# Kernel optimization log

Hardware: AMD Instinct MI355X
Metric: run time of the kernel (lower is better)

## Reference

```python
import jax, jax.numpy as jnp
import numpy as np

B, T, C = 4, 4096, 1024


def setup_inputs() -> dict:
    key = jax.random.key(0)
    k_x, k_f, k_g, k_p = jax.random.split(key, 4)
    scale = 1.0 / np.sqrt(C)  # keep gate pre-activations well-scaled
    return {
        "x": jax.random.normal(k_x, (B, T, C), dtype=jnp.float32),
        "W_f_x": jax.random.normal(k_f, (C, C), dtype=jnp.float32) * scale,
        "W_g_x": jax.random.normal(k_g, (C, C), dtype=jnp.float32) * scale,
        "W_proj": jax.random.normal(k_p, (C, C), dtype=jnp.float32) * scale,
    }


def _cfc_scan(a, b):
    """Solve h_t = a_t * h_{t-1} + b_t with h_{-1}=0 along axis 1 (T).

    Associative op on linear maps: (A_l,B_l) then (A_r,B_r) composes to
    (A_r*A_l, A_r*B_l + B_r). With h_init=0, h_t = B-component.
    """
    def op(l, r):
        al, bl = l
        ar, br = r
        return ar * al, ar * bl + br
    _, h = jax.lax.associative_scan(op, (a, b), axis=1)
    return h


def reference(x, W_f_x, W_g_x, W_proj):
    # Gates depend on x only (parallel mode). nn.Linear: x @ W.T
    f = jax.nn.sigmoid(jnp.einsum("btc,dc->btd", x, W_f_x))  # (B,T,C)
    g = jnp.tanh(jnp.einsum("btc,dc->btd", x, W_g_x))        # (B,T,C)
    h = _cfc_scan(f, (1.0 - f) * g)                           # (B,T,C)
    return jnp.einsum("btc,dc->btd", h, W_proj)               # c_proj
```

## Files before the change

kernel.cpp:

```cpp
#include <hip/hip_runtime.h>
#include <hip/hip_bf16.h>
#include <stdint.h>

#define TT 4096
#define BB 4
#define CC 1024
#define MM (BB * TT)
#define NCHUNK 128
#define CHUNK_T (TT / NCHUNK)
#define NCHAIN (BB * CC)

typedef float f32x4 __attribute__((ext_vector_type(4)));
typedef __bf16 bf16x8 __attribute__((ext_vector_type(8)));

__device__ __forceinline__ float b2f(ushort u) {
  union { float f; uint32_t v; } x; x.v = ((uint32_t)u) << 16; return x.f;
}
__device__ __forceinline__ ushort f2b(float f) {
  union { float f; uint32_t u; } x; x.f = f;
  uint32_t r = x.u + 0x7fffu + ((x.u >> 16) & 1u);
  return (ushort)(r >> 16);
}

__device__ __forceinline__ void async_copy16(const ushort* g, ushort* l) {
  __builtin_amdgcn_global_load_lds(
      (__attribute__((address_space(1))) void*)(g),
      (__attribute__((address_space(3))) void*)(l), 16, 0, 0);
}

__global__ __launch_bounds__(256) void cvt_all(const float* __restrict__ x,
                                               const float* __restrict__ wf,
                                               const float* __restrict__ wg,
                                               const float* __restrict__ wp,
                                               ushort* __restrict__ xb,
                                               ushort* __restrict__ wcat,
                                               ushort* __restrict__ wpb) {
  const int i = blockIdx.x * 256 + threadIdx.x;
  const float* s; ushort* d; int off;
  if (i < 4194304)            { s = x;  d = xb;              off = i; }
  else if (i < 4456448)       { s = wf; d = wcat;            off = i - 4194304; }
  else if (i < 4718592)       { s = wg; d = wcat + 1048576;  off = i - 4456448; }
  else                        { s = wp; d = wpb;             off = i - 4718592; }
  float4 v = ((const float4*)s)[off];
  ushort4 o;
  o.x = f2b(v.x); o.y = f2b(v.y); o.z = f2b(v.z); o.w = f2b(v.w);
  ((ushort4*)d)[off] = o;
}


#define RDA(sl, ih)                                                       \
  _Pragma("unroll") for (int i_ = 0; i_ < 4; ++i_)                        \
      af[i_] = *(const bf16x8*)(rA + (sl) * 8192 + (ih) * 2048 + i_ * 512);

#define RDB(sl)                                                           \
  _Pragma("unroll") for (int j_ = 0; j_ < 4; ++j_)                        \
      bfr[j_] = *(const bf16x8*)(rB + (sl) * 8192 + j_ * 512);

#define MFMA16(ih)                                                        \
  __builtin_amdgcn_s_setprio(1);                                          \
  _Pragma("unroll") for (int i_ = 0; i_ < 4; ++i_)                        \
  _Pragma("unroll") for (int j_ = 0; j_ < 4; ++j_)                        \
      acc[(ih) * 4 + i_][j_] = __builtin_amdgcn_mfma_f32_16x16x32_bf16(   \
          bfr[j_], af[i_], acc[(ih) * 4 + i_][j_], 0, 0, 0);              \
  __builtin_amdgcn_s_setprio(0)

#define MIDBAR()                                                          \
  __builtin_amdgcn_s_barrier();                                           \
  asm volatile("s_waitcnt lgkmcnt(0)" ::: "memory");                      \
  __builtin_amdgcn_sched_barrier(0)

#define ENDBAR()                                                          \
  __builtin_amdgcn_s_barrier();                                           \
  __builtin_amdgcn_sched_barrier(0)

#define CK4() asm volatile("s_waitcnt vmcnt(4)" ::: "memory")
#define CK0() asm volatile("s_waitcnt vmcnt(0)" ::: "memory")

#define TILE(S0, S1, NS0, NS1, KN)                                        \
  RDA(S0, 0); RDB(S0); stageA(NS0, (KN));      MIDBAR(); MFMA16(0);        ENDBAR(); \
  RDA(S0, 1);          stageB(NS0, (KN));      MIDBAR(); MFMA16(1); CK4(); ENDBAR(); \
  RDA(S1, 0); RDB(S1); stageA(NS1, (KN) + 32); MIDBAR(); MFMA16(0);        ENDBAR(); \
  RDA(S1, 1);          stageB(NS1, (KN) + 32); MIDBAR(); MFMA16(1); CK4(); ENDBAR();

template <int MODE>
__global__ __launch_bounds__(512, 2) void gemm_bt(const ushort* __restrict__ A,
                                                  const ushort* __restrict__ Bw,
                                                  float* __restrict__ outF,
                                                  ushort* __restrict__ outB, int N) {
  constexpr int K = CC;
  __shared__ __align__(16) ushort sA[4 * 256 * 32];
  __shared__ __align__(16) ushort sB[4 * 256 * 32];

  const int tid = threadIdx.x;
  const int lane = tid & 63;
  const int w = tid >> 6;
  const int wm = w >> 2;
  const int wn = w & 3;

  const int nbx = N >> 8;
  const int cpx = (int)gridDim.x >> 3;
  const int bid = blockIdx.x;
  const int wg = (bid & 7) * cpx + (bid >> 3);
  const long n0 = (long)(wg % nbx) << 8;
  const long m0 = (long)(wg / nbx) << 8;

  const int srow = lane >> 2;
  const int goct = (lane & 3) ^ ((lane >> 3) & 3);
  const ushort* gA0 = A + (m0 + w * 16 + srow) * K + goct * 8;
  const ushort* gB0 = Bw + (n0 + w * 16 + srow) * K + goct * 8;
  const ushort* gA1 = gA0 + 128 * (long)K;
  const ushort* gB1 = gB0 + 128 * (long)K;
  ushort* dA0 = &sA[w * 512 + lane * 8];
  ushort* dA1 = dA0 + 4096;
  ushort* dB0 = &sB[w * 512 + lane * 8];
  ushort* dB1 = dB0 + 4096;

  auto stageA = [&](int slot, int koff) {
    async_copy16(gA0 + koff, dA0 + slot * 8192);
    async_copy16(gA1 + koff, dA1 + slot * 8192);
  };
  auto stageB = [&](int slot, int koff) {
    async_copy16(gB0 + koff, dB0 + slot * 8192);
    async_copy16(gB1 + koff, dB1 + slot * 8192);
  };

  const int rlo = lane & 15;
  const int kq = lane >> 4;
  const int oslot = kq ^ ((rlo >> 1) & 3);
  const ushort* rA = &sA[(wm * 128 + rlo) * 32 + oslot * 8];
  const ushort* rB = &sB[(wn * 64 + rlo) * 32 + oslot * 8];

  f32x4 acc[8][4];
#pragma unroll
  for (int i = 0; i < 8; ++i)
#pragma unroll
    for (int j = 0; j < 4; ++j) acc[i][j] = (f32x4){0.f, 0.f, 0.f, 0.f};

  bf16x8 af[4], bfr[4];

  stageA(0, 0);
  stageB(0, 0);
  stageA(1, 32);
  stageB(1, 32);
  CK4();
  ENDBAR();

  for (int t2 = 0; t2 < 7; ++t2) {
    const int kn = t2 * 128 + 64;
    TILE(0, 1, 2, 3, kn);
    TILE(2, 3, 0, 1, kn + 64);
  }
  TILE(0, 1, 2, 3, 960);
  RDA(2, 0); RDB(2); MIDBAR(); MFMA16(0); ENDBAR();
  RDA(2, 1);         MIDBAR(); MFMA16(1); CK0(); ENDBAR();
  RDA(3, 0); RDB(3); MIDBAR(); MFMA16(0); ENDBAR();
  RDA(3, 1);         MIDBAR(); MFMA16(1);

  const int mloc = lane & 15;
  const int nq = (lane >> 4) * 4;
#pragma unroll
  for (int i = 0; i < 8; ++i) {
    const long m = m0 + wm * 128 + i * 16 + mloc;
#pragma unroll
    for (int j = 0; j < 4; ++j) {
      const long nb = n0 + wn * 64 + j * 16 + nq;
      const f32x4 v = acc[i][j];
      if (MODE == 0) {
        *(f32x4*)(outF + m * N + nb) = v;
      } else {
        float act[4];
        if (n0 < CC) {
#pragma unroll
          for (int r = 0; r < 4; ++r)
            act[r] = __builtin_amdgcn_rcpf(1.f + __expf(-v[r]));
        } else {
#pragma unroll
          for (int r = 0; r < 4; ++r)
            act[r] = fmaf(-2.f, __builtin_amdgcn_rcpf(1.f + __expf(2.f * v[r])), 1.f);
        }
        ushort4 o;
        o.x = f2b(act[0]); o.y = f2b(act[1]); o.z = f2b(act[2]); o.w = f2b(act[3]);
        *(ushort4*)(outB + m * (long)N + nb) = o;
      }
    }
  }
}

__global__ __launch_bounds__(256) void scan_pass1(const ushort* __restrict__ P,
                                                  float* __restrict__ cA,
                                                  float* __restrict__ cB) {
  const int pc = blockIdx.x * 256 + threadIdx.x;
  const int chunk = blockIdx.y;
  const int b = pc >> 8, c4 = (pc & 255) * 4;
  const ushort4* p =
      (const ushort4*)(P + (size_t)(b * TT + chunk * CHUNK_T) * (2 * CC) + c4);
  float A[4] = {1.f, 1.f, 1.f, 1.f};
  float h[4] = {0.f, 0.f, 0.f, 0.f};
#pragma unroll 4
  for (int i = 0; i < CHUNK_T; ++i) {
    const ushort4 fu = p[0];
    const ushort4 gu = p[CC / 4];
    p += 2 * CC / 4;
    const float f[4] = {b2f(fu.x), b2f(fu.y), b2f(fu.z), b2f(fu.w)};
    const float g[4] = {b2f(gu.x), b2f(gu.y), b2f(gu.z), b2f(gu.w)};
#pragma unroll
    for (int r = 0; r < 4; ++r) {
      A[r] *= f[r];
      h[r] = fmaf(f[r], h[r], (1.f - f[r]) * g[r]);
    }
  }
  const int ci = chunk * NCHAIN + b * CC + c4;
  *(f32x4*)(cA + ci) = (f32x4){A[0], A[1], A[2], A[3]};
  *(f32x4*)(cB + ci) = (f32x4){h[0], h[1], h[2], h[3]};
}

__global__ __launch_bounds__(256) void scan_pass2(const float* __restrict__ cA,
                                                  const float* __restrict__ cB,
                                                  float* __restrict__ hinit) {
  const int chain = blockIdx.x * 256 + threadIdx.x;
  float h = 0.f;
  for (int j = 0; j < NCHUNK; ++j) {
    hinit[j * NCHAIN + chain] = h;
    h = fmaf(cA[j * NCHAIN + chain], h, cB[j * NCHAIN + chain]);
  }
}

__global__ __launch_bounds__(256) void scan_pass3(const ushort* __restrict__ P,
                                                  const float* __restrict__ hinit,
                                                  ushort* __restrict__ H) {
  const int pc = blockIdx.x * 256 + threadIdx.x;
  const int chunk = blockIdx.y;
  const int b = pc >> 8, c4 = (pc & 255) * 4;
  f32x4 hv = *(const f32x4*)(hinit + chunk * NCHAIN + b * CC + c4);
  float h[4] = {hv[0], hv[1], hv[2], hv[3]};
  const ushort4* p =
      (const ushort4*)(P + (size_t)(b * TT + chunk * CHUNK_T) * (2 * CC) + c4);
  ushort4* hp = (ushort4*)(H + (size_t)(b * TT + chunk * CHUNK_T) * CC + c4);
#pragma unroll 4
  for (int i = 0; i < CHUNK_T; ++i) {
    const ushort4 fu = p[0];
    const ushort4 gu = p[CC / 4];
    p += 2 * CC / 4;
    const float f[4] = {b2f(fu.x), b2f(fu.y), b2f(fu.z), b2f(fu.w)};
    const float g[4] = {b2f(gu.x), b2f(gu.y), b2f(gu.z), b2f(gu.w)};
    ushort4 o;
#pragma unroll
    for (int r = 0; r < 4; ++r)
      h[r] = fmaf(f[r], h[r], (1.f - f[r]) * g[r]);
    o.x = f2b(h[0]); o.y = f2b(h[1]); o.z = f2b(h[2]); o.w = f2b(h[3]);
    *hp = o;
    hp += CC / 4;
  }
}

extern "C" void kernel_launch(void* const* d_in, const int* in_sizes, int n_in,
                              void* d_out, int out_size, void* d_ws, size_t ws_size,
                              hipStream_t stream) {
  const float* x  = (const float*)d_in[0];
  const float* Wf = (const float*)d_in[1];
  const float* Wg = (const float*)d_in[2];
  const float* Wp = (const float*)d_in[3];

  char* ws = (char*)d_ws;
  ushort* xb   = (ushort*)(ws);
  ushort* Hb   = xb;
  ushort* Wcat = (ushort*)(ws + 33554432);
  ushort* Wpb  = (ushort*)(ws + 33554432 + 4194304);
  ushort* P    = (ushort*)(ws + 33554432 + 4194304 + 2097152);
  char* tail   = ws + 33554432 + 4194304 + 2097152 + 67108864;
  float* cA    = (float*)Wcat;
  float* cB    = (float*)(((char*)Wcat) + 2097152);
  float* hinit = (float*)(tail);
  (void)ws_size; (void)in_sizes; (void)n_in; (void)out_size;

  cvt_all<<<19456, 256, 0, stream>>>(x, Wf, Wg, Wp, xb, Wcat, Wpb);

  gemm_bt<1><<<512, 512, 0, stream>>>(xb, Wcat, nullptr, P, 2 * CC);

  dim3 gs(NCHAIN / 4 / 256, NCHUNK);
  scan_pass1<<<gs, 256, 0, stream>>>(P, cA, cB);
  scan_pass2<<<NCHAIN / 256, 256, 0, stream>>>(cA, cB, hinit);
  scan_pass3<<<gs, 256, 0, stream>>>(P, hinit, Hb);

  gemm_bt<0><<<256, 512, 0, stream>>>(Hb, Wpb, (float*)d_out, nullptr, CC);
}
```

Before: 280.7 us.

## Fuse chunk scan summaries into gate GEMM epilogue with interleaved f/g layout

Interleaves the f and g weight rows so each GEMM output tile holds matching f/g pairs per channel. The GEMM epilogue then computes per-chunk (A,B) scan summaries via wave shuffles, which removes the separate scan_pass1 read of the full gate tensor. pass2 becomes a 64-lane shuffle scan over chunks, and pass3 reads the interleaved f/g pairs with one 16-byte load. The cost is a heavier GEMM epilogue with many shuffles and strided small stores of the summaries.

After: 269.9 us. -3.8%, faster.

```diff
diff --git a/kernel.cpp b/kernel.cpp
--- a/kernel.cpp
+++ b/kernel.cpp
@@ -6,12 +6,13 @@
 #define BB 4
 #define CC 1024
 #define MM (BB * TT)
-#define NCHUNK 128
+#define NCHUNK 64
 #define CHUNK_T (TT / NCHUNK)
 #define NCHAIN (BB * CC)
 
 typedef float f32x4 __attribute__((ext_vector_type(4)));
 typedef __bf16 bf16x8 __attribute__((ext_vector_type(8)));
+typedef ushort us8 __attribute__((ext_vector_type(8)));
 
 __device__ __forceinline__ float b2f(ushort u) {
   union { float f; uint32_t v; } x; x.v = ((uint32_t)u) << 16; return x.f;
@@ -36,15 +37,22 @@
                                                ushort* __restrict__ wcat,
                                                ushort* __restrict__ wpb) {
   const int i = blockIdx.x * 256 + threadIdx.x;
-  const float* s; ushort* d; int off;
-  if (i < 4194304)            { s = x;  d = xb;              off = i; }
-  else if (i < 4456448)       { s = wf; d = wcat;            off = i - 4194304; }
-  else if (i < 4718592)       { s = wg; d = wcat + 1048576;  off = i - 4456448; }
-  else                        { s = wp; d = wpb;             off = i - 4718592; }
+  const float* s; ushort* d; int off, dst;
+  if (i < 4194304) {
+    s = x; d = xb; off = i; dst = i;
+  } else if (i < 4456448) {
+    s = wf; d = wcat; off = i - 4194304;
+    dst = ((off >> 8) << 9) + (off & 255);
+  } else if (i < 4718592) {
+    s = wg; d = wcat; off = i - 4456448;
+    dst = ((off >> 8) << 9) + 256 + (off & 255);
+  } else {
+    s = wp; d = wpb; off = i - 4718592; dst = off;
+  }
   float4 v = ((const float4*)s)[off];
   ushort4 o;
   o.x = f2b(v.x); o.y = f2b(v.y); o.z = f2b(v.z); o.w = f2b(v.w);
-  ((ushort4*)d)[off] = o;
+  ((ushort4*)d)[dst] = o;
 }
 
 
@@ -82,11 +90,21 @@
   RDA(S1, 0); RDB(S1); stageA(NS1, (KN) + 32); MIDBAR(); MFMA16(0);        ENDBAR(); \
   RDA(S1, 1);          stageB(NS1, (KN) + 32); MIDBAR(); MFMA16(1); CK4(); ENDBAR();
 
+#define BFLY16(Av, Bv)                                                    \
+  _Pragma("unroll") for (int m_ = 1; m_ < 16; m_ <<= 1) {                 \
+    float Ao_ = __shfl_xor(Av, m_);                                       \
+    float Bo_ = __shfl_xor(Bv, m_);                                       \
+    Bv = ((lane & m_) == 0) ? fmaf(Ao_, Bv, Bo_) : fmaf(Av, Bo_, Bv);     \
+    Av = Ao_ * Av;                                                        \
+  }
+
 template <int MODE>
 __global__ __launch_bounds__(512, 2) void gemm_bt(const ushort* __restrict__ A,
                                                   const ushort* __restrict__ Bw,
                                                   float* __restrict__ outF,
-                                                  ushort* __restrict__ outB, int N) {
+                                                  ushort* __restrict__ outB,
+                                                  float* __restrict__ cA2,
+                                                  float* __restrict__ cB2, int N) {
   constexpr int K = CC;
   __shared__ __align__(16) ushort sA[4 * 256 * 32];
   __shared__ __align__(16) ushort sB[4 * 256 * 32];
@@ -158,95 +176,110 @@
 
   const int mloc = lane & 15;
   const int nq = (lane >> 4) * 4;
-#pragma unroll
-  for (int i = 0; i < 8; ++i) {
-    const long m = m0 + wm * 128 + i * 16 + mloc;
-#pragma unroll
-    for (int j = 0; j < 4; ++j) {
-      const long nb = n0 + wn * 64 + j * 16 + nq;
-      const f32x4 v = acc[i][j];
-      if (MODE == 0) {
-        *(f32x4*)(outF + m * N + nb) = v;
-      } else {
-        float act[4];
-        if (n0 < CC) {
-#pragma unroll
-          for (int r = 0; r < 4; ++r)
-            act[r] = __builtin_amdgcn_rcpf(1.f + __expf(-v[r]));
-        } else {
-#pragma unroll
-          for (int r = 0; r < 4; ++r)
-            act[r] = fmaf(-2.f, __builtin_amdgcn_rcpf(1.f + __expf(2.f * v[r])), 1.f);
-        }
-        ushort4 o;
-        o.x = f2b(act[0]); o.y = f2b(act[1]); o.z = f2b(act[2]); o.w = f2b(act[3]);
-        *(ushort4*)(outB + m * (long)N + nb) = o;
+
+  if (MODE == 0) {
+#pragma unroll
+    for (int i = 0; i < 8; ++i) {
+      const long m = m0 + wm * 128 + i * 16 + mloc;
+#pragma unroll
+      for (int j = 0; j < 4; ++j) {
+        const long nb = n0 + wn * 64 + j * 16 + nq;
+        *(f32x4*)(outF + m * N + nb) = acc[i][j];
       }
     }
-  }
-}
-
-__global__ __launch_bounds__(256) void scan_pass1(const ushort* __restrict__ P,
-                                                  float* __restrict__ cA,
-                                                  float* __restrict__ cB) {
-  const int pc = blockIdx.x * 256 + threadIdx.x;
-  const int chunk = blockIdx.y;
-  const int b = pc >> 8, c4 = (pc & 255) * 4;
-  const ushort4* p =
-      (const ushort4*)(P + (size_t)(b * TT + chunk * CHUNK_T) * (2 * CC) + c4);
-  float A[4] = {1.f, 1.f, 1.f, 1.f};
-  float h[4] = {0.f, 0.f, 0.f, 0.f};
-#pragma unroll 4
-  for (int i = 0; i < CHUNK_T; ++i) {
-    const ushort4 fu = p[0];
-    const ushort4 gu = p[CC / 4];
-    p += 2 * CC / 4;
-    const float f[4] = {b2f(fu.x), b2f(fu.y), b2f(fu.z), b2f(fu.w)};
-    const float g[4] = {b2f(gu.x), b2f(gu.y), b2f(gu.z), b2f(gu.w)};
-#pragma unroll
-    for (int r = 0; r < 4; ++r) {
-      A[r] *= f[r];
-      h[r] = fmaf(f[r], h[r], (1.f - f[r]) * g[r]);
+  } else {
+    const int kq4 = lane >> 4;
+    const long bIdx = m0 >> 12;
+    const int t0 = (int)(m0 & 4095) + wm * 128;
+    const long chb = (n0 >> 1) + wn * 32;
+#pragma unroll
+    for (int cp = 0; cp < 2; ++cp) {
+      float CA[4][2], CB[4][2];
+#pragma unroll
+      for (int hh = 0; hh < 4; ++hh) {
+        const int i = cp * 4 + hh;
+        const long m = m0 + wm * 128 + i * 16 + mloc;
+#pragma unroll
+        for (int j = 0; j < 4; ++j) {
+          const long nb = n0 + wn * 64 + j * 16 + nq;
+          const f32x4 v = acc[i][j];
+          float act0 = __builtin_amdgcn_rcpf(1.f + __expf(-v[0]));
+          float act1 = fmaf(-2.f, __builtin_amdgcn_rcpf(1.f + __expf(2.f * v[1])), 1.f);
+          float act2 = __builtin_amdgcn_rcpf(1.f + __expf(-v[2]));
+          float act3 = fmaf(-2.f, __builtin_amdgcn_rcpf(1.f + __expf(2.f * v[3])), 1.f);
+          ushort4 o;
+          o.x = f2b(act0); o.y = f2b(act1); o.z = f2b(act2); o.w = f2b(act3);
+          *(ushort4*)(outB + m * (long)N + nb) = o;
+          const float fr0 = b2f(o.x), gr0 = b2f(o.y);
+          const float fr1 = b2f(o.z), gr1 = b2f(o.w);
+          float a0 = fr0, b0 = (1.f - fr0) * gr0;
+          float a1 = fr1, b1 = (1.f - fr1) * gr1;
+          BFLY16(a0, b0);
+          BFLY16(a1, b1);
+          if (hh == 0) {
+            CA[j][0] = a0; CB[j][0] = b0;
+            CA[j][1] = a1; CB[j][1] = b1;
+          } else {
+            CB[j][0] = fmaf(a0, CB[j][0], b0); CA[j][0] *= a0;
+            CB[j][1] = fmaf(a1, CB[j][1], b1); CA[j][1] *= a1;
+          }
+        }
+      }
+      if (mloc == 0) {
+        const int gchunk = (t0 >> 6) + cp;
+#pragma unroll
+        for (int j = 0; j < 4; ++j) {
+          const long ch0 = chb + j * 8 + kq4 * 2;
+          const long i0 = (bIdx * CC + ch0) * 64 + gchunk;
+          cA2[i0] = CA[j][0];       cB2[i0] = CB[j][0];
+          cA2[i0 + 64] = CA[j][1];  cB2[i0 + 64] = CB[j][1];
+        }
+      }
     }
   }
-  const int ci = chunk * NCHAIN + b * CC + c4;
-  *(f32x4*)(cA + ci) = (f32x4){A[0], A[1], A[2], A[3]};
-  *(f32x4*)(cB + ci) = (f32x4){h[0], h[1], h[2], h[3]};
-}
-
-__global__ __launch_bounds__(256) void scan_pass2(const float* __restrict__ cA,
-                                                  const float* __restrict__ cB,
-                                                  float* __restrict__ hinit) {
-  const int chain = blockIdx.x * 256 + threadIdx.x;
-  float h = 0.f;
-  for (int j = 0; j < NCHUNK; ++j) {
-    hinit[j * NCHAIN + chain] = h;
-    h = fmaf(cA[j * NCHAIN + chain], h, cB[j * NCHAIN + chain]);
-  }
+}
+
+__global__ __launch_bounds__(256) void scan_pass2(const float* __restrict__ cA2,
+                                                  const float* __restrict__ cB2,
+                                                  float* __restrict__ h2) {
+  const int gid = blockIdx.x * 256 + threadIdx.x;
+  const int chain = gid >> 6;
+  const int lane = threadIdx.x & 63;
+  float Av = cA2[chain * 64 + lane];
+  float Bv = cB2[chain * 64 + lane];
+#pragma unroll
+  for (int m = 1; m < 64; m <<= 1) {
+    const float Ao = __shfl_up(Av, m);
+    const float Bo = __shfl_up(Bv, m);
+    if (lane >= m) { Bv = fmaf(Av, Bo, Bv); Av = Av * Ao; }
+  }
+  const float Bx = __shfl_up(Bv, 1);
+  h2[chain * 64 + lane] = (lane == 0) ? 0.f : Bx;
 }
 
 __global__ __launch_bounds__(256) void scan_pass3(const ushort* __restrict__ P,
-                                                  const float* __restrict__ hinit,
+                                                  const float* __restrict__ h2,
                                                   ushort* __restrict__ H) {
   const int pc = blockIdx.x * 256 + threadIdx.x;
   const int chunk = blockIdx.y;
   const int b = pc >> 8, c4 = (pc & 255) * 4;
-  f32x4 hv = *(const f32x4*)(hinit + chunk * NCHAIN + b * CC + c4);
-  float h[4] = {hv[0], hv[1], hv[2], hv[3]};
-  const ushort4* p =
-      (const ushort4*)(P + (size_t)(b * TT + chunk * CHUNK_T) * (2 * CC) + c4);
+  float h[4];
+#pragma unroll
+  for (int r = 0; r < 4; ++r) h[r] = h2[(b * CC + c4 + r) * 64 + chunk];
+  const us8* p =
+      (const us8*)(P + (size_t)(b * TT + chunk * CHUNK_T) * (2 * CC) + c4 * 2);
   ushort4* hp = (ushort4*)(H + (size_t)(b * TT + chunk * CHUNK_T) * CC + c4);
 #pragma unroll 4
   for (int i = 0; i < CHUNK_T; ++i) {
-    const ushort4 fu = p[0];
-    const ushort4 gu = p[CC / 4];
-    p += 2 * CC / 4;
-    const float f[4] = {b2f(fu.x), b2f(fu.y), b2f(fu.z), b2f(fu.w)};
-    const float g[4] = {b2f(gu.x), b2f(gu.y), b2f(gu.z), b2f(gu.w)};
+    const us8 v = p[0];
+    p += 2 * CC / 8;
     ushort4 o;
 #pragma unroll
-    for (int r = 0; r < 4; ++r)
-      h[r] = fmaf(f[r], h[r], (1.f - f[r]) * g[r]);
+    for (int r = 0; r < 4; ++r) {
+      const float f = b2f(v[2 * r]);
+      const float g = b2f(v[2 * r + 1]);
+      h[r] = fmaf(f, h[r], (1.f - f) * g);
+    }
     o.x = f2b(h[0]); o.y = f2b(h[1]); o.z = f2b(h[2]); o.w = f2b(h[3]);
     *hp = o;
     hp += CC / 4;
@@ -268,19 +301,18 @@
   ushort* Wpb  = (ushort*)(ws + 33554432 + 4194304);
   ushort* P    = (ushort*)(ws + 33554432 + 4194304 + 2097152);
   char* tail   = ws + 33554432 + 4194304 + 2097152 + 67108864;
-  float* cA    = (float*)Wcat;
-  float* cB    = (float*)(((char*)Wcat) + 2097152);
-  float* hinit = (float*)(tail);
+  float* cA2   = (float*)(tail);
+  float* cB2   = (float*)(tail + 1048576);
+  float* h2    = (float*)(tail + 2097152);
   (void)ws_size; (void)in_sizes; (void)n_in; (void)out_size;
 
   cvt_all<<<19456, 256, 0, stream>>>(x, Wf, Wg, Wp, xb, Wcat, Wpb);
 
-  gemm_bt<1><<<512, 512, 0, stream>>>(xb, Wcat, nullptr, P, 2 * CC);
-
+  gemm_bt<1><<<512, 512, 0, stream>>>(xb, Wcat, nullptr, P, cA2, cB2, 2 * CC);
+
+  scan_pass2<<<NCHAIN * 64 / 256, 256, 0, stream>>>(cA2, cB2, h2);
   dim3 gs(NCHAIN / 4 / 256, NCHUNK);
-  scan_pass1<<<gs, 256, 0, stream>>>(P, cA, cB);
-  scan_pass2<<<NCHAIN / 256, 256, 0, stream>>>(cA, cB, hinit);
-  scan_pass3<<<gs, 256, 0, stream>>>(P, hinit, Hb);
-
-  gemm_bt<0><<<256, 512, 0, stream>>>(Hb, Wpb, (float*)d_out, nullptr, CC);
-}
+  scan_pass3<<<gs, 256, 0, stream>>>(P, h2, Hb);
+
+  gemm_bt<0><<<256, 512, 0, stream>>>(Hb, Wpb, (float*)d_out, nullptr, nullptr, nullptr, CC);
+}
```
